# Performance work log

Measured on AMD Instinct MI355X. Metric: run time of the kernel, lower is better.

Reference implementation:

```python
import jax, jax.numpy as jnp
import numpy as np

N, L, S, D = 8, 1024, 4096, 512
EPS = 1e-5

def layernorm(x, g, b):
    mu = jnp.mean(x, axis=-1, keepdims=True)
    var = jnp.var(x, axis=-1, keepdims=True)
    return (x - mu) * jax.lax.rsqrt(var + EPS) * g + b

def setup_inputs() -> dict:
    key = jax.random.key(0)
    ks = jax.random.split(key, 8)
    w = lambda k, shp: jax.random.normal(k, shp, dtype=jnp.float32) * 0.02
    return {
        "x": jax.random.normal(ks[0], (N, L, D), dtype=jnp.float32),
        "source": jax.random.normal(ks[1], (N, S, D), dtype=jnp.float32),
        "Wq": w(ks[2], (D, D)),
        "Wk": w(ks[3], (D, D)),
        "Wv": w(ks[4], (D, D)),
        "Wm": w(ks[5], (D, D)),
        "W1": w(ks[6], (2 * D, 2 * D)),
        "W2": w(ks[7], (2 * D, D)),
        "g1": jnp.ones((D,), jnp.float32),
        "b1": jnp.zeros((D,), jnp.float32),
        "g2": jnp.ones((D,), jnp.float32),
        "b2": jnp.zeros((D,), jnp.float32),
    }

def reference(x, source, Wq, Wk, Wv, Wm, W1, W2, g1, b1, g2, b2):
    # projections
    q = x @ Wq          # [N, L, D]
    k = source @ Wk     # [N, S, D]
    v = source @ Wv     # [N, S, D]
    # pairwise L2 distance via ||q||^2 + ||k||^2 - 2 q.k (avoids [N,L,S,D] tensor)
    q2 = jnp.sum(q * q, axis=-1)                      # [N, L]
    k2 = jnp.sum(k * k, axis=-1)                      # [N, S]
    qk = jnp.einsum('nlc,nsc->nls', q, k)             # [N, L, S]
    dist = jnp.sqrt(jnp.maximum(q2[:, :, None] + k2[:, None, :] - 2.0 * qk, 0.0))
    attn = jax.nn.softmax(dist, axis=2)               # softmax over S (note: +distance, as in source)
    message = jnp.einsum('nls,nsc->nlc', attn, v)     # [N, L, D]
    message = layernorm(message @ Wm, g1, b1)
    h = jnp.concatenate([x, message], axis=2)         # [N, L, 2D]
    message = jax.nn.relu(h @ W1) @ W2                # [N, L, D]
    message = layernorm(message, g2, b2)
    return x + message
```

## Files before the change

### kernel.cpp

```cpp
#include <hip/hip_runtime.h>
#include <stdint.h>

typedef unsigned short u16;
typedef __attribute__((ext_vector_type(8))) short bf16x8;
typedef __attribute__((ext_vector_type(4))) float f32x4;
typedef __attribute__((ext_vector_type(4))) unsigned int u32x4;

__device__ __forceinline__ u16 f2b(float f) {
  uint32_t u = __float_as_uint(f);
  u += 0x7fffu + ((u >> 16) & 1u);
  return (u16)(u >> 16);
}
__device__ __forceinline__ float b2f(u16 h) {
  return __uint_as_float(((uint32_t)h) << 16);
}
__device__ __forceinline__ uint32_t pack2bf(float a, float b) {
#if __has_builtin(__builtin_amdgcn_cvt_pk_bf16_f32)
  typedef __attribute__((ext_vector_type(2))) __bf16 bf16x2_t;
  bf16x2_t r = __builtin_amdgcn_cvt_pk_bf16_f32(a, b);
  return __builtin_bit_cast(uint32_t, r);
#else
  return (uint32_t)f2b(a) | ((uint32_t)f2b(b) << 16);
#endif
}

__device__ __forceinline__ void gload_lds16(const u16* g, u16* l) {
  __builtin_amdgcn_global_load_lds(
      (const __attribute__((address_space(1))) void*)g,
      (__attribute__((address_space(3))) void*)l, 16, 0, 0);
}

enum { EPI_BF16_T = 0, EPI_BF16_T_SQ = 1, EPI_F32_T = 2, EPI_RELU_BF16_T = 3,
       EPI_EXP_T = 4 };

template <int EPI>
__device__ __forceinline__ void gemm_body(
    u16* smem, const u16* A, size_t sA, int lda,
    const u16* B, size_t sB, int ldb,
    void* C, size_t sC, int ldc, int K, size_t pStride,
    const float* e_col2, const float* e_row2, float* e_l,
    int lin, int gx, int gy) {
  u16* As = smem;
  u16* Bs = smem + 8192;
  const int t = threadIdx.x;
  const int batch = lin & 7;
  const int rest = lin >> 3;
  const int bx = rest % gx;
  const int ry = rest / gx;
  const int by = ry % gy;
  const int part = ry / gy;
  const int m0 = by * 128, n0 = bx * 128;
  const int koff = part * K;
  const u16* Ab = A + (size_t)batch * sA + (size_t)m0 * lda + koff;
  const u16* Bb = B + (size_t)batch * sB + (size_t)n0 * ldb + koff;
  const int srow = t >> 3;
  const int skey = (srow & 3) | (((srow >> 3) & 1) << 2);
  const int scol = ((t & 7) ^ skey) << 3;
  const u16* aS = Ab + (size_t)srow * lda + scol;
  const u16* bS = Bb + (size_t)srow * ldb + scol;
  const size_t a32 = (size_t)32 * lda, b32 = (size_t)32 * ldb;
  u16* asDst = As + t * 8;
  u16* bsDst = Bs + t * 8;

  const int w = t >> 6, lane = t & 63;
  const int wm = (w >> 1) << 6, wn = (w & 1) << 6;
  const int qd = lane >> 4, l16 = lane & 15;
  const int rbase = ((l16 >> 2) << 3) + (l16 & 3);
  const int keyA = (l16 & 3) | (((l16 >> 2) & 1) << 2);
  const int keyB = (l16 & 3) | (((l16 >> 3) & 1) << 2);
  const u16* aRow0 = As + (wm + rbase) * 64;
  const u16* bRow0 = Bs + (wn + l16) * 64;

  f32x4 acc[4][4];
#pragma unroll
  for (int i = 0; i < 4; i++)
#pragma unroll
    for (int j = 0; j < 4; j++) acc[i][j] = (f32x4)0.0f;

  for (int k0 = 0; k0 < K; k0 += 64) {
    gload_lds16(aS, asDst);
    gload_lds16(aS + a32, asDst + 2048);
    gload_lds16(aS + 2 * a32, asDst + 4096);
    gload_lds16(aS + 3 * a32, asDst + 6144);
    gload_lds16(bS, bsDst);
    gload_lds16(bS + b32, bsDst + 2048);
    gload_lds16(bS + 2 * b32, bsDst + 4096);
    gload_lds16(bS + 3 * b32, bsDst + 6144);
    aS += 64;
    bS += 64;
    __syncthreads();
#pragma unroll
    for (int s = 0; s < 2; s++) {
      const int ca = (((qd | (s << 2)) ^ keyA) << 3);
      const int cb = (((qd | (s << 2)) ^ keyB) << 3);
      bf16x8 af[4], bfr[4];
      af[0] = *(const bf16x8*)(aRow0 + ca);
      af[1] = *(const bf16x8*)(aRow0 + 4 * 64 + ca);
      af[2] = *(const bf16x8*)(aRow0 + 32 * 64 + ca);
      af[3] = *(const bf16x8*)(aRow0 + 36 * 64 + ca);
#pragma unroll
      for (int i = 0; i < 4; i++)
        bfr[i] = *(const bf16x8*)(bRow0 + i * 16 * 64 + cb);
#pragma unroll
      for (int mi = 0; mi < 4; mi++)
#pragma unroll
        for (int ni = 0; ni < 4; ni++)
          acc[mi][ni] = __builtin_amdgcn_mfma_f32_16x16x32_bf16(
              af[mi], bfr[ni], acc[mi][ni], 0, 0, 0);
    }
    __syncthreads();
  }

  const size_t cbase = (size_t)part * pStride + (size_t)batch * sC;
  const int ncols = (int)(sC / ldc);

  if constexpr (EPI == EPI_EXP_T) {
    const int nrows = (int)(sA / lda);
    const float* col2 = e_col2 + (size_t)batch * ncols;
    const float* row2 = e_row2 + (size_t)batch * nrows;
    float* lb = e_l + (size_t)batch * ncols;
    float c2v[4];
#pragma unroll
    for (int ni = 0; ni < 4; ni++) c2v[ni] = col2[n0 + wn + ni * 16 + l16];
    float cs[4] = {0.f, 0.f, 0.f, 0.f};
#pragma unroll
    for (int p = 0; p < 2; p++) {
      const int prow = m0 + wm + p * 32 + qd * 8;
      float r2v[8];
#pragma unroll
      for (int r8 = 0; r8 < 8; r8++) r2v[r8] = row2[prow + r8];
#pragma unroll
      for (int ni = 0; ni < 4; ni++) {
        const int col = n0 + wn + ni * 16 + l16;
        float pv[8];
#pragma unroll
        for (int r = 0; r < 4; r++) {
          pv[r] = __expf(sqrtf(
              fmaxf(c2v[ni] + r2v[r] - 2.0f * acc[2 * p][ni][r], 0.0f)));
          pv[4 + r] = __expf(sqrtf(
              fmaxf(c2v[ni] + r2v[4 + r] - 2.0f * acc[2 * p + 1][ni][r], 0.0f)));
        }
#pragma unroll
        for (int j = 0; j < 8; j++) cs[ni] += pv[j];
        u32x4 wv;
        wv[0] = pack2bf(pv[0], pv[1]);
        wv[1] = pack2bf(pv[2], pv[3]);
        wv[2] = pack2bf(pv[4], pv[5]);
        wv[3] = pack2bf(pv[6], pv[7]);
        *(u32x4*)((u16*)C + cbase + (size_t)col * ldc + prow) = wv;
      }
    }
#pragma unroll
    for (int ni = 0; ni < 4; ni++) {
      cs[ni] += __shfl_xor(cs[ni], 16);
      cs[ni] += __shfl_xor(cs[ni], 32);
    }
    if (qd == 0) {
#pragma unroll
      for (int ni = 0; ni < 4; ni++)
        atomicAdd(lb + n0 + wn + ni * 16 + l16, cs[ni]);
    }
  } else if constexpr (EPI == EPI_F32_T) {
#pragma unroll
    for (int p = 0; p < 2; p++) {
      const int prow = m0 + wm + p * 32 + qd * 8;
#pragma unroll
      for (int ni = 0; ni < 4; ni++) {
        const int col = n0 + wn + ni * 16 + l16;
        float* dst = (float*)C + cbase + (size_t)col * ldc + prow;
        *(f32x4*)dst = acc[2 * p][ni];
        *(f32x4*)(dst + 4) = acc[2 * p + 1][ni];
      }
    }
  } else {
    float cs[4] = {0.f, 0.f, 0.f, 0.f};
#pragma unroll
    for (int p = 0; p < 2; p++) {
      const int prow = m0 + wm + p * 32 + qd * 8;
#pragma unroll
      for (int ni = 0; ni < 4; ni++) {
        const int col = n0 + wn + ni * 16 + l16;
        float v[8];
#pragma unroll
        for (int r = 0; r < 4; r++) {
          v[r] = acc[2 * p][ni][r];
          v[4 + r] = acc[2 * p + 1][ni][r];
        }
        if (EPI == EPI_RELU_BF16_T) {
#pragma unroll
          for (int j = 0; j < 8; j++) v[j] = fmaxf(v[j], 0.0f);
        }
        if (EPI == EPI_BF16_T_SQ) {
#pragma unroll
          for (int j = 0; j < 8; j++) cs[ni] += v[j] * v[j];
        }
        u32x4 wv;
        wv[0] = pack2bf(v[0], v[1]);
        wv[1] = pack2bf(v[2], v[3]);
        wv[2] = pack2bf(v[4], v[5]);
        wv[3] = pack2bf(v[6], v[7]);
        *(u32x4*)((u16*)C + cbase + (size_t)col * ldc + prow) = wv;
      }
    }
    if (EPI == EPI_BF16_T_SQ) {
#pragma unroll
      for (int ni = 0; ni < 4; ni++) {
        cs[ni] += __shfl_xor(cs[ni], 16);
        cs[ni] += __shfl_xor(cs[ni], 32);
      }
      if (qd == 0) {
#pragma unroll
        for (int ni = 0; ni < 4; ni++)
          atomicAdd(e_l + (size_t)batch * ncols + n0 + wn + ni * 16 + l16,
                    cs[ni]);
      }
    }
  }
}

template <int EPI>
__global__ __launch_bounds__(256, 2) void gemm_nt(
    const u16* __restrict__ A, size_t sA, int lda,
    const u16* __restrict__ B, size_t sB, int ldb,
    void* __restrict__ C, size_t sC, int ldc, int K, size_t pStride,
    const float* __restrict__ e_col2, const float* __restrict__ e_row2,
    float* __restrict__ e_l) {
  __shared__ __align__(16) u16 smem[16384];
  const int lin = blockIdx.x + gridDim.x * (blockIdx.y + gridDim.y * blockIdx.z);
  gemm_body<EPI>(smem, A, sA, lda, B, sB, ldb, C, sC, ldc, K, pStride,
                 e_col2, e_row2, e_l, lin, gridDim.x, gridDim.y);
}

__global__ __launch_bounds__(256, 2) void proj_fused(
    const u16* __restrict__ WqT, const u16* __restrict__ WkT,
    const u16* __restrict__ WvT, const u16* __restrict__ h,
    const u16* __restrict__ sb, u16* __restrict__ q, u16* __restrict__ kb,
    u16* __restrict__ vT, float* __restrict__ q2, float* __restrict__ k2) {
  __shared__ __align__(16) u16 smem[16384];
  const int lin = blockIdx.x;
  if (lin < 256) {
    gemm_body<EPI_BF16_T_SQ>(smem, WqT, 0, 512, h, (size_t)1024 * 1024, 1024,
                             q, (size_t)1024 * 512, 512, 512, 0, nullptr,
                             nullptr, q2, lin, 8, 4);
  } else if (lin < 1280) {
    gemm_body<EPI_BF16_T_SQ>(smem, WkT, 0, 512, sb, (size_t)4096 * 512, 512,
                             kb, (size_t)4096 * 512, 512, 512, 0, nullptr,
                             nullptr, k2, lin - 256, 32, 4);
  } else {
    gemm_body<EPI_BF16_T>(smem, sb, (size_t)4096 * 512, 512, WvT, 0, 512,
                          vT, (size_t)512 * 4096, 4096, 512, 0, nullptr,
                          nullptr, nullptr, lin - 1280, 4, 32);
  }
}

__global__ __launch_bounds__(256) void reduce2_div_bf16(
    const float* __restrict__ P, const float* __restrict__ l,
    u16* __restrict__ out) {
  const size_t i = (size_t)blockIdx.x * 256 + threadIdx.x;
  const float4* p = (const float4*)P;
  float4 a = p[i];
  float4 b = p[i + 1048576];
  const float inv = 1.0f / l[i >> 7];
  ushort4 o = make_ushort4(f2b((a.x + b.x) * inv), f2b((a.y + b.y) * inv),
                           f2b((a.z + b.z) * inv), f2b((a.w + b.w) * inv));
  *(ushort4*)(out + (i << 2)) = o;
}

__global__ __launch_bounds__(256) void fused_prep(
    const float* __restrict__ x, const float* __restrict__ sc,
    u16* __restrict__ h, u16* __restrict__ sb, float* __restrict__ q2,
    float* __restrict__ k2, float* __restrict__ lsum) {
  const size_t i = (size_t)blockIdx.x * 256 + threadIdx.x;
  if (i < 1048576) {
    const float4 f = ((const float4*)x)[i];
    const int e = (int)(i << 2);
    const int row = e >> 9, col = e & 511;
    *(ushort4*)(h + ((size_t)row << 10) + col) =
        make_ushort4(f2b(f.x), f2b(f.y), f2b(f.z), f2b(f.w));
  } else if (i < 5242880) {
    const size_t j = i - 1048576;
    const float4 f = ((const float4*)sc)[j];
    *(ushort4*)(sb + (j << 2)) =
        make_ushort4(f2b(f.x), f2b(f.y), f2b(f.z), f2b(f.w));
  } else {
    const size_t j = i - 5242880;
    const float4 z = {0.f, 0.f, 0.f, 0.f};
    if (j < 2048) ((float4*)q2)[j] = z;
    else if (j < 10240) ((float4*)k2)[j - 2048] = z;
    else ((float4*)lsum)[j - 10240] = z;
  }
}

__global__ void transpose_w6(
    const float* __restrict__ Wq, const float* __restrict__ Wk,
    const float* __restrict__ Wv, const float* __restrict__ Wm,
    const float* __restrict__ W1, const float* __restrict__ W2,
    u16* __restrict__ WqT, u16* __restrict__ WkT, u16* __restrict__ WvT,
    u16* __restrict__ WmT, u16* __restrict__ W1T, u16* __restrict__ W2T) {
  __shared__ float tile[32][33];
  const float* W;
  u16* WT;
  int R, Cn;
  switch (blockIdx.z) {
    case 0: W = Wq; WT = WqT; R = 512; Cn = 512; break;
    case 1: W = Wk; WT = WkT; R = 512; Cn = 512; break;
    case 2: W = Wv; WT = WvT; R = 512; Cn = 512; break;
    case 3: W = Wm; WT = WmT; R = 512; Cn = 512; break;
    case 4: W = W1; WT = W1T; R = 1024; Cn = 1024; break;
    default: W = W2; WT = W2T; R = 1024; Cn = 512; break;
  }
  const int c0 = blockIdx.x * 32, r0 = blockIdx.y * 32;
  if (c0 >= Cn || r0 >= R) return;
  const int tx = threadIdx.x, ty = threadIdx.y;
  for (int i = ty; i < 32; i += 8) tile[i][tx] = W[(size_t)(r0 + i) * Cn + c0 + tx];
  __syncthreads();
  for (int i = ty; i < 32; i += 8) WT[(size_t)(c0 + i) * R + r0 + tx] = f2b(tile[tx][i]);
}

__global__ __launch_bounds__(128) void ln_to_h(const float* __restrict__ mm,
                                               const float* __restrict__ g,
                                               const float* __restrict__ b,
                                               u16* __restrict__ h) {
  const size_t row = blockIdx.x;
  const int t = threadIdx.x;
  const float4 f = ((const float4*)(mm + row * 512))[t];
  float s = f.x + f.y + f.z + f.w;
  float sq = f.x * f.x + f.y * f.y + f.z * f.z + f.w * f.w;
#pragma unroll
  for (int off = 32; off; off >>= 1) { s += __shfl_xor(s, off); sq += __shfl_xor(sq, off); }
  __shared__ float rs_[2], rq_[2];
  if ((t & 63) == 0) { rs_[t >> 6] = s; rq_[t >> 6] = sq; }
  __syncthreads();
  s = rs_[0] + rs_[1]; sq = rq_[0] + rq_[1];
  const float mu = s * (1.0f / 512.0f);
  const float rstd = rsqrtf(sq * (1.0f / 512.0f) - mu * mu + 1e-5f);
  const float4 gv = ((const float4*)g)[t], bv = ((const float4*)b)[t];
  ushort4 o = make_ushort4(f2b((f.x - mu) * rstd * gv.x + bv.x),
                           f2b((f.y - mu) * rstd * gv.y + bv.y),
                           f2b((f.z - mu) * rstd * gv.z + bv.z),
                           f2b((f.w - mu) * rstd * gv.w + bv.w));
  *(ushort4*)(h + (row << 10) + 512 + (t << 2)) = o;
}

__global__ __launch_bounds__(128) void ln_residual(const float* __restrict__ m2,
                                                   const float* __restrict__ x,
                                                   const float* __restrict__ g,
                                                   const float* __restrict__ b,
                                                   float* __restrict__ out) {
  const size_t row = blockIdx.x;
  const int t = threadIdx.x;
  const float4 f = ((const float4*)(m2 + row * 512))[t];
  float s = f.x + f.y + f.z + f.w;
  float sq = f.x * f.x + f.y * f.y + f.z * f.z + f.w * f.w;
#pragma unroll
  for (int off = 32; off; off >>= 1) { s += __shfl_xor(s, off); sq += __shfl_xor(sq, off); }
  __shared__ float rs_[2], rq_[2];
  if ((t & 63) == 0) { rs_[t >> 6] = s; rq_[t >> 6] = sq; }
  __syncthreads();
  s = rs_[0] + rs_[1]; sq = rq_[0] + rq_[1];
  const float mu = s * (1.0f / 512.0f);
  const float rstd = rsqrtf(sq * (1.0f / 512.0f) - mu * mu + 1e-5f);
  const float4 gv = ((const float4*)g)[t], bv = ((const float4*)b)[t];
  const float4 xv = ((const float4*)(x + row * 512))[t];
  float4 o;
  o.x = xv.x + (f.x - mu) * rstd * gv.x + bv.x;
  o.y = xv.y + (f.y - mu) * rstd * gv.y + bv.y;
  o.z = xv.z + (f.z - mu) * rstd * gv.z + bv.z;
  o.w = xv.w + (f.w - mu) * rstd * gv.w + bv.w;
  ((float4*)(out + row * 512))[t] = o;
}

extern "C" void kernel_launch(void* const* d_in, const int* in_sizes, int n_in,
                              void* d_out, int out_size, void* d_ws, size_t ws_size,
                              hipStream_t stream) {
  const float* x  = (const float*)d_in[0];
  const float* sc = (const float*)d_in[1];
  const float* Wq = (const float*)d_in[2];
  const float* Wk = (const float*)d_in[3];
  const float* Wv = (const float*)d_in[4];
  const float* Wm = (const float*)d_in[5];
  const float* W1 = (const float*)d_in[6];
  const float* W2 = (const float*)d_in[7];
  const float* g1 = (const float*)d_in[8];
  const float* b1 = (const float*)d_in[9];
  const float* g2 = (const float*)d_in[10];
  const float* b2 = (const float*)d_in[11];
  float* out = (float*)d_out;
  char* ws = (char*)d_ws;

  constexpr int N = 8, L = 1024, S = 4096, D = 512;
  u16*   h   = (u16*)(ws + 0);
  u16*   sb  = (u16*)(ws + 16777216);
  u16*   WqT = (u16*)(ws + 50331648);
  u16*   WkT = (u16*)(ws + 50855936);
  u16*   WvT = (u16*)(ws + 51380224);
  u16*   WmT = (u16*)(ws + 51904512);
  u16*   W1T = (u16*)(ws + 52428800);
  u16*   W2T = (u16*)(ws + 54525952);
  u16*   q   = (u16*)(ws + 55574528);
  u16*   kb  = (u16*)(ws + 63963136);
  u16*   vT  = (u16*)(ws + 97517568);
  float* lsum= (float*)(ws + 131072000);
  float* q2  = (float*)(ws + 164626432);
  float* k2  = (float*)(ws + 164659200);
  u16*   qk  = (u16*)(ws + 164790272);
  u16*   msg = (u16*)(ws + 55574528);
  float* mpart = (float*)(ws + 63963136);
  float* mm  = (float*)(ws + 63963136);
  u16*   hh  = (u16*)(ws + 80740352);
  float* m2  = (float*)(ws + 97517568);

  fused_prep<<<dim3(20528), 256, 0, stream>>>(x, sc, h, sb, q2, k2, lsum);
  transpose_w6<<<dim3(32, 32, 6), dim3(32, 8), 0, stream>>>(
      Wq, Wk, Wv, Wm, W1, W2, WqT, WkT, WvT, WmT, W1T, W2T);

  proj_fused<<<dim3(2304), 256, 0, stream>>>(WqT, WkT, WvT, h, sb, q, kb, vT,
                                             q2, k2);

  gemm_nt<EPI_EXP_T><<<dim3(8, 32, 8), 256, 0, stream>>>(
      kb, (size_t)S * 512, 512, q, (size_t)L * 512, 512, qk, (size_t)L * S, S,
      512, 0, q2, k2, lsum);
  gemm_nt<EPI_F32_T><<<dim3(8, 4, 16), 256, 0, stream>>>(
      vT, (size_t)D * S, S, qk, (size_t)L * S, S, mpart, (size_t)L * 512, 512,
      2048, (size_t)(N * L) * 512, nullptr, nullptr, nullptr);
  reduce2_div_bf16<<<dim3(4096), 256, 0, stream>>>(mpart, lsum, msg);

  gemm_nt<EPI_F32_T><<<dim3(8, 4, 8), 256, 0, stream>>>(
      WmT, 0, 512, msg, (size_t)L * 512, 512, mm, (size_t)L * 512, 512, 512, 0,
      nullptr, nullptr, nullptr);
  ln_to_h<<<dim3(N * L), 128, 0, stream>>>(mm, g1, b1, h);

  gemm_nt<EPI_RELU_BF16_T><<<dim3(8, 8, 8), 256, 0, stream>>>(
      W1T, 0, 1024, h, (size_t)L * 1024, 1024, hh, (size_t)L * 1024, 1024, 1024,
      0, nullptr, nullptr, nullptr);
  gemm_nt<EPI_F32_T><<<dim3(8, 4, 8), 256, 0, stream>>>(
      W2T, 0, 1024, hh, (size_t)L * 1024, 1024, m2, (size_t)L * 512, 512, 1024,
      0, nullptr, nullptr, nullptr);

  ln_residual<<<dim3(N * L), 128, 0, stream>>>(m2, x, g2, b2, out);
}
```

Before: 373.7 us.

## Add 256x256-tile 512-thread GEMM with double-buffered LDS for projections and distance-exp

Adds a new GEMM body using 256x256 output tiles, 8 waves, 128 KB of dynamic LDS double buffering, and interleaved async global-to-LDS staging with explicit vmcnt waits, barriers and s_setprio around the MFMA bursts. The fused Q/K/V projection kernel and the distance/exp/softmax-numerator GEMM move to this kernel; the old 128x128 exp epilogue and proj_fused are removed. The aim is higher arithmetic intensity and overlap of loads with MFMA. In exchange it uses far fewer, larger blocks with heavy register and LDS use, so occupancy drops and tail effects may grow.

```diff
diff --git a/kernel.cpp b/kernel.cpp
--- a/kernel.cpp
+++ b/kernel.cpp
@@ -32,6 +32,250 @@
 
 enum { EPI_BF16_T = 0, EPI_BF16_T_SQ = 1, EPI_F32_T = 2, EPI_RELU_BF16_T = 3,
        EPI_EXP_T = 4 };
+
+
+#define VMW4 asm volatile("s_waitcnt vmcnt(4)" ::: "memory")
+#define VMW0 asm volatile("s_waitcnt vmcnt(0)" ::: "memory")
+#define BARX()                                   \
+  do {                                           \
+    asm volatile("" ::: "memory");               \
+    __builtin_amdgcn_s_barrier();                \
+    asm volatile("" ::: "memory");               \
+  } while (0)
+
+#define STG_A(tl, kh, j)                                                  \
+  gload_lds16(aSrc + (size_t)(j) * 128 * lda + (tl) * 64 + (kh) * 32,     \
+              aDst + ((tl) & 1) * 16384 + (kh) * 8192 + (j) * 4096)
+#define STG_B(tl, kh, j)                                                  \
+  gload_lds16(bSrc + (size_t)(j) * 128 * ldb + (tl) * 64 + (kh) * 32,     \
+              bDst + ((tl) & 1) * 16384 + (kh) * 8192 + (j) * 4096)
+
+#define LDA4(kh, g)                                                       \
+  do {                                                                    \
+    const u16* ap_ = smem + cb * 16384 + (kh) * 8192 + aoff + (g) * 2048; \
+    af[0] = *(const bf16x8*)(ap_);                                        \
+    af[1] = *(const bf16x8*)(ap_ + 128);                                  \
+    af[2] = *(const bf16x8*)(ap_ + 1024);                                 \
+    af[3] = *(const bf16x8*)(ap_ + 1152);                                 \
+  } while (0)
+#define LDB4(kh)                                                          \
+  do {                                                                    \
+    const u16* bp_ = smem + cb * 16384 + (kh) * 8192 + boff;              \
+    bf[0] = *(const bf16x8*)(bp_);                                        \
+    bf[1] = *(const bf16x8*)(bp_ + 512);                                  \
+    bf[2] = *(const bf16x8*)(bp_ + 1024);                                 \
+    bf[3] = *(const bf16x8*)(bp_ + 1536);                                 \
+  } while (0)
+#define MF16(g)                                                           \
+  do {                                                                    \
+    __builtin_amdgcn_s_setprio(1);                                        \
+    _Pragma("unroll") for (int i_ = 0; i_ < 4; i_++)                      \
+        _Pragma("unroll") for (int n_ = 0; n_ < 4; n_++)                  \
+            acc[(g) * 4 + i_][n_] = __builtin_amdgcn_mfma_f32_16x16x32_bf16( \
+                af[i_], bf[n_], acc[(g) * 4 + i_][n_], 0, 0, 0);          \
+    __builtin_amdgcn_s_setprio(0);                                        \
+  } while (0)
+
+template <int EPI>
+__device__ __forceinline__ void gemm256_body(
+    u16* smem, const u16* A, size_t sA, int lda,
+    const u16* B, size_t sB, int ldb,
+    void* C, size_t sC, int ldc, int K,
+    const float* e_col2, const float* e_row2, float* e_l,
+    int lin, int gx) {
+  const int t = threadIdx.x;
+  const int batch = lin & 7;
+  const int rest = lin >> 3;
+  const int bx = rest % gx;
+  const int by = rest / gx;
+  const int m0 = by << 8, n0 = bx << 8;
+  const u16* Ab = A + (size_t)batch * sA + (size_t)m0 * lda;
+  const u16* Bb = B + (size_t)batch * sB + (size_t)n0 * ldb;
+  const u16* aSrc = Ab + (size_t)(t >> 2) * lda + ((t & 3) << 3);
+  const u16* bSrc = Bb + (size_t)(t >> 2) * ldb + ((t & 3) << 3);
+  u16* aDst = smem + t * 8;
+  u16* bDst = smem + 32768 + t * 8;
+
+  const int w = t >> 6, lane = t & 63;
+  const int wr = w >> 2, wc = w & 3;
+  const int qd = lane >> 4, l16 = lane & 15;
+  const int rbase = ((l16 >> 2) << 3) + (l16 & 3);
+  const int aoff = (wr * 128 + rbase) * 32 + qd * 8;
+  const int boff = 32768 + (wc * 64 + l16) * 32 + qd * 8;
+  const int nt = K >> 6;
+
+  f32x4 acc[8][4];
+#pragma unroll
+  for (int i = 0; i < 8; i++)
+#pragma unroll
+    for (int j = 0; j < 4; j++) acc[i][j] = (f32x4)0.0f;
+
+  STG_A(0, 0, 0); STG_A(0, 0, 1);
+  STG_B(0, 0, 0); STG_B(0, 0, 1);
+  STG_A(0, 1, 0); STG_A(0, 1, 1);
+  STG_B(0, 1, 0); STG_B(0, 1, 1);
+  VMW4;
+  BARX();
+
+#pragma unroll 2
+  for (int tt = 0; tt < nt; ++tt) {
+    const int cb = tt & 1;
+    const bool pre = (tt + 1) < nt;
+    bf16x8 af[4], bf[4];
+    LDA4(0, 0);
+    LDB4(0);
+    if (pre) { STG_A(tt + 1, 0, 0); STG_A(tt + 1, 0, 1); }
+    BARX();
+    MF16(0);
+    BARX();
+    LDA4(0, 1);
+    if (pre) { STG_B(tt + 1, 0, 0); STG_B(tt + 1, 0, 1); VMW4; }
+    else { VMW0; }
+    BARX();
+    MF16(1);
+    BARX();
+    LDA4(1, 0);
+    LDB4(1);
+    if (pre) { STG_A(tt + 1, 1, 0); STG_A(tt + 1, 1, 1); }
+    BARX();
+    MF16(0);
+    BARX();
+    LDA4(1, 1);
+    if (pre) { STG_B(tt + 1, 1, 0); STG_B(tt + 1, 1, 1); VMW4; }
+    BARX();
+    MF16(1);
+    BARX();
+  }
+
+  const int colb = n0 + wc * 64;
+  const size_t cbase = (size_t)batch * sC;
+  if constexpr (EPI == EPI_EXP_T) {
+    const int ncols = (int)(sC / ldc);
+    const int nrows = (int)(sA / lda);
+    const float* col2 = e_col2 + (size_t)batch * ncols;
+    const float* row2 = e_row2 + (size_t)batch * nrows;
+    float* lb = e_l + (size_t)batch * ncols;
+    float c2v[4], cs[4] = {0.f, 0.f, 0.f, 0.f};
+#pragma unroll
+    for (int n = 0; n < 4; n++) c2v[n] = col2[colb + n * 16 + l16];
+#pragma unroll
+    for (int g = 0; g < 2; g++)
+#pragma unroll
+      for (int p2 = 0; p2 < 2; p2++) {
+        const int prow = m0 + wr * 128 + g * 64 + p2 * 32 + qd * 8;
+        const int mb = g * 4 + p2 * 2;
+        float r2v[8];
+#pragma unroll
+        for (int r8 = 0; r8 < 8; r8++) r2v[r8] = row2[prow + r8];
+#pragma unroll
+        for (int n = 0; n < 4; n++) {
+          float pv[8];
+#pragma unroll
+          for (int r = 0; r < 4; r++) {
+            pv[r] = __expf(sqrtf(
+                fmaxf(c2v[n] + r2v[r] - 2.0f * acc[mb][n][r], 0.0f)));
+            pv[4 + r] = __expf(sqrtf(
+                fmaxf(c2v[n] + r2v[4 + r] - 2.0f * acc[mb + 1][n][r], 0.0f)));
+          }
+#pragma unroll
+          for (int j = 0; j < 8; j++) cs[n] += pv[j];
+          u32x4 wv;
+          wv[0] = pack2bf(pv[0], pv[1]);
+          wv[1] = pack2bf(pv[2], pv[3]);
+          wv[2] = pack2bf(pv[4], pv[5]);
+          wv[3] = pack2bf(pv[6], pv[7]);
+          *(u32x4*)((u16*)C + cbase + (size_t)(colb + n * 16 + l16) * ldc +
+                    prow) = wv;
+        }
+      }
+#pragma unroll
+    for (int n = 0; n < 4; n++) {
+      cs[n] += __shfl_xor(cs[n], 16);
+      cs[n] += __shfl_xor(cs[n], 32);
+    }
+    if (qd == 0) {
+#pragma unroll
+      for (int n = 0; n < 4; n++)
+        atomicAdd(lb + colb + n * 16 + l16, cs[n]);
+    }
+  } else {
+    float cs[4] = {0.f, 0.f, 0.f, 0.f};
+#pragma unroll
+    for (int g = 0; g < 2; g++)
+#pragma unroll
+      for (int p2 = 0; p2 < 2; p2++) {
+        const int prow = m0 + wr * 128 + g * 64 + p2 * 32 + qd * 8;
+        const int mb = g * 4 + p2 * 2;
+#pragma unroll
+        for (int n = 0; n < 4; n++) {
+          float v[8];
+#pragma unroll
+          for (int r = 0; r < 4; r++) {
+            v[r] = acc[mb][n][r];
+            v[4 + r] = acc[mb + 1][n][r];
+          }
+          if (EPI == EPI_BF16_T_SQ) {
+#pragma unroll
+            for (int j = 0; j < 8; j++) cs[n] += v[j] * v[j];
+          }
+          u32x4 wv;
+          wv[0] = pack2bf(v[0], v[1]);
+          wv[1] = pack2bf(v[2], v[3]);
+          wv[2] = pack2bf(v[4], v[5]);
+          wv[3] = pack2bf(v[6], v[7]);
+          *(u32x4*)((u16*)C + cbase + (size_t)(colb + n * 16 + l16) * ldc +
+                    prow) = wv;
+        }
+      }
+    if (EPI == EPI_BF16_T_SQ) {
+      const int ncols = (int)(sC / ldc);
+#pragma unroll
+      for (int n = 0; n < 4; n++) {
+        cs[n] += __shfl_xor(cs[n], 16);
+        cs[n] += __shfl_xor(cs[n], 32);
+      }
+      if (qd == 0) {
+#pragma unroll
+        for (int n = 0; n < 4; n++)
+          atomicAdd(e_l + (size_t)batch * ncols + colb + n * 16 + l16, cs[n]);
+      }
+    }
+  }
+}
+
+template <int EPI>
+__global__ __launch_bounds__(512, 2) void gemm256_nt(
+    const u16* __restrict__ A, size_t sA, int lda,
+    const u16* __restrict__ B, size_t sB, int ldb,
+    void* __restrict__ C, size_t sC, int ldc, int K, int gx,
+    const float* __restrict__ e_col2, const float* __restrict__ e_row2,
+    float* __restrict__ e_l) {
+  extern __shared__ u16 smem[];
+  gemm256_body<EPI>(smem, A, sA, lda, B, sB, ldb, C, sC, ldc, K,
+                    e_col2, e_row2, e_l, blockIdx.x, gx);
+}
+
+__global__ __launch_bounds__(512, 2) void proj256_fused(
+    const u16* __restrict__ WqT, const u16* __restrict__ WkT,
+    const u16* __restrict__ WvT, const u16* __restrict__ h,
+    const u16* __restrict__ sb, u16* __restrict__ q, u16* __restrict__ kb,
+    u16* __restrict__ vT, float* __restrict__ q2, float* __restrict__ k2) {
+  extern __shared__ u16 smem[];
+  const int lin = blockIdx.x;
+  if (lin < 256) {
+    gemm256_body<EPI_BF16_T_SQ>(smem, WkT, 0, 512, sb, (size_t)4096 * 512,
+                                512, kb, (size_t)4096 * 512, 512, 512,
+                                nullptr, nullptr, k2, lin, 16);
+  } else if (lin < 512) {
+    gemm256_body<EPI_BF16_T>(smem, sb, (size_t)4096 * 512, 512, WvT, 0, 512,
+                             vT, (size_t)512 * 4096, 4096, 512,
+                             nullptr, nullptr, nullptr, lin - 256, 2);
+  } else {
+    gemm256_body<EPI_BF16_T_SQ>(smem, WqT, 0, 512, h, (size_t)1024 * 1024,
+                                1024, q, (size_t)1024 * 512, 512, 512,
+                                nullptr, nullptr, q2, lin - 512, 4);
+  }
+}
 
 template <int EPI>
 __device__ __forceinline__ void gemm_body(
@@ -114,53 +358,7 @@
   const size_t cbase = (size_t)part * pStride + (size_t)batch * sC;
   const int ncols = (int)(sC / ldc);
 
-  if constexpr (EPI == EPI_EXP_T) {
-    const int nrows = (int)(sA / lda);
-    const float* col2 = e_col2 + (size_t)batch * ncols;
-    const float* row2 = e_row2 + (size_t)batch * nrows;
-    float* lb = e_l + (size_t)batch * ncols;
-    float c2v[4];
-#pragma unroll
-    for (int ni = 0; ni < 4; ni++) c2v[ni] = col2[n0 + wn + ni * 16 + l16];
-    float cs[4] = {0.f, 0.f, 0.f, 0.f};
-#pragma unroll
-    for (int p = 0; p < 2; p++) {
-      const int prow = m0 + wm + p * 32 + qd * 8;
-      float r2v[8];
-#pragma unroll
-      for (int r8 = 0; r8 < 8; r8++) r2v[r8] = row2[prow + r8];
-#pragma unroll
-      for (int ni = 0; ni < 4; ni++) {
-        const int col = n0 + wn + ni * 16 + l16;
-        float pv[8];
-#pragma unroll
-        for (int r = 0; r < 4; r++) {
-          pv[r] = __expf(sqrtf(
-              fmaxf(c2v[ni] + r2v[r] - 2.0f * acc[2 * p][ni][r], 0.0f)));
-          pv[4 + r] = __expf(sqrtf(
-              fmaxf(c2v[ni] + r2v[4 + r] - 2.0f * acc[2 * p + 1][ni][r], 0.0f)));
-        }
-#pragma unroll
-        for (int j = 0; j < 8; j++) cs[ni] += pv[j];
-        u32x4 wv;
-        wv[0] = pack2bf(pv[0], pv[1]);
-        wv[1] = pack2bf(pv[2], pv[3]);
-        wv[2] = pack2bf(pv[4], pv[5]);
-        wv[3] = pack2bf(pv[6], pv[7]);
-        *(u32x4*)((u16*)C + cbase + (size_t)col * ldc + prow) = wv;
-      }
-    }
-#pragma unroll
-    for (int ni = 0; ni < 4; ni++) {
-      cs[ni] += __shfl_xor(cs[ni], 16);
-      cs[ni] += __shfl_xor(cs[ni], 32);
-    }
-    if (qd == 0) {
-#pragma unroll
-      for (int ni = 0; ni < 4; ni++)
-        atomicAdd(lb + n0 + wn + ni * 16 + l16, cs[ni]);
-    }
-  } else if constexpr (EPI == EPI_F32_T) {
+  if constexpr (EPI == EPI_F32_T) {
 #pragma unroll
     for (int p = 0; p < 2; p++) {
       const int prow = m0 + wm + p * 32 + qd * 8;
@@ -229,28 +427,6 @@
   const int lin = blockIdx.x + gridDim.x * (blockIdx.y + gridDim.y * blockIdx.z);
   gemm_body<EPI>(smem, A, sA, lda, B, sB, ldb, C, sC, ldc, K, pStride,
                  e_col2, e_row2, e_l, lin, gridDim.x, gridDim.y);
-}
-
-__global__ __launch_bounds__(256, 2) void proj_fused(
-    const u16* __restrict__ WqT, const u16* __restrict__ WkT,
-    const u16* __restrict__ WvT, const u16* __restrict__ h,
-    const u16* __restrict__ sb, u16* __restrict__ q, u16* __restrict__ kb,
-    u16* __restrict__ vT, float* __restrict__ q2, float* __restrict__ k2) {
-  __shared__ __align__(16) u16 smem[16384];
-  const int lin = blockIdx.x;
-  if (lin < 256) {
-    gemm_body<EPI_BF16_T_SQ>(smem, WqT, 0, 512, h, (size_t)1024 * 1024, 1024,
-                             q, (size_t)1024 * 512, 512, 512, 0, nullptr,
-                             nullptr, q2, lin, 8, 4);
-  } else if (lin < 1280) {
-    gemm_body<EPI_BF16_T_SQ>(smem, WkT, 0, 512, sb, (size_t)4096 * 512, 512,
-                             kb, (size_t)4096 * 512, 512, 512, 0, nullptr,
-                             nullptr, k2, lin - 256, 32, 4);
-  } else {
-    gemm_body<EPI_BF16_T>(smem, sb, (size_t)4096 * 512, 512, WvT, 0, 512,
-                          vT, (size_t)512 * 4096, 4096, 512, 0, nullptr,
-                          nullptr, nullptr, lin - 1280, 4, 32);
-  }
 }
 
 __global__ __launch_bounds__(256) void reduce2_div_bf16(
@@ -414,12 +590,12 @@
   transpose_w6<<<dim3(32, 32, 6), dim3(32, 8), 0, stream>>>(
       Wq, Wk, Wv, Wm, W1, W2, WqT, WkT, WvT, WmT, W1T, W2T);
 
-  proj_fused<<<dim3(2304), 256, 0, stream>>>(WqT, WkT, WvT, h, sb, q, kb, vT,
-                                             q2, k2);
-
-  gemm_nt<EPI_EXP_T><<<dim3(8, 32, 8), 256, 0, stream>>>(
+  proj256_fused<<<dim3(576), 512, 131072, stream>>>(WqT, WkT, WvT, h, sb, q,
+                                                    kb, vT, q2, k2);
+
+  gemm256_nt<EPI_EXP_T><<<dim3(512), 512, 131072, stream>>>(
       kb, (size_t)S * 512, 512, q, (size_t)L * 512, 512, qk, (size_t)L * S, S,
-      512, 0, q2, k2, lsum);
+      512, 4, q2, k2, lsum);
   gemm_nt<EPI_F32_T><<<dim3(8, 4, 16), 256, 0, stream>>>(
       vT, (size_t)D * S, S, qk, (size_t)L * S, S, mpart, (size_t)L * 512, 512,
       2048, (size_t)(N * L) * 512, nullptr, nullptr, nullptr);
```

After: 398.3 us. 6.6% more time.
